# Kernel tuning notes

Hardware: AMD Instinct MI355X
Metric: run time of the kernel (lower is better)

## Reference

```python
import jax, jax.numpy as jnp
import numpy as np

N_NODES = 100000
N_EDGES = 400000
N_GRAPHS = 2048
F_IN = 78
HEADS1 = 10
OUT2 = 128


def _gat_conv(x, src, dst, W, a_src, a_dst, b, heads, out_dim):
    """PyG-style GATConv with self-loops already included in (src, dst)."""
    N = x.shape[0]
    h = (x @ W).reshape(N, heads, out_dim)                       # [N,H,D]
    alpha_src = jnp.einsum('nhd,hd->nh', h, a_src)               # [N,H]
    alpha_dst = jnp.einsum('nhd,hd->nh', h, a_dst)               # [N,H]
    e = jax.nn.leaky_relu(alpha_src[src] + alpha_dst[dst], 0.2)  # [E,H]
    # ragged softmax over incoming edges per destination node
    m = jax.ops.segment_max(e, dst, num_segments=N)
    m = jnp.where(jnp.isfinite(m), m, 0.0)
    ex = jnp.exp(e - jax.lax.stop_gradient(m)[dst])
    denom = jax.ops.segment_sum(ex, dst, num_segments=N)
    alpha = ex / (denom[dst] + 1e-16)                            # [E,H]
    msg = h[src] * alpha[:, :, None]                             # [E,H,D]
    out = jax.ops.segment_sum(msg, dst, num_segments=N)          # [N,H,D]
    return out.reshape(N, heads * out_dim) + b


def setup_inputs() -> dict:
    key = jax.random.key(0)
    ks = jax.random.split(key, 24)
    p = lambda k, shape: (jax.random.normal(k, shape, dtype=jnp.float32) * 0.05)
    x = jax.random.normal(ks[0], (N_NODES, F_IN), dtype=jnp.float32)
    edge_index = jax.random.randint(ks[1], (2, N_EDGES), 0, N_NODES, dtype=jnp.int32)
    # sorted batch assignment guaranteeing every graph is non-empty
    batch = ((jnp.arange(N_NODES, dtype=jnp.int32) * N_GRAPHS) // N_NODES).astype(jnp.int32)
    target = jax.random.normal(ks[2], (N_GRAPHS, 1280), dtype=jnp.float32)
    return {
        'x': x, 'edge_index': edge_index, 'batch': batch, 'target': target,
        'W1': p(ks[3], (F_IN, HEADS1 * F_IN)),
        'a_src1': p(ks[4], (HEADS1, F_IN)),
        'a_dst1': p(ks[5], (HEADS1, F_IN)),
        'b1': jnp.zeros((HEADS1 * F_IN,), jnp.float32),
        'W2': p(ks[6], (HEADS1 * F_IN, OUT2)),
        'a_src2': p(ks[7], (1, OUT2)),
        'a_dst2': p(ks[8], (1, OUT2)),
        'b2': jnp.zeros((OUT2,), jnp.float32),
        'w_gate': p(ks[9], (OUT2, 1)),
        'b_gate': jnp.zeros((1,), jnp.float32),
        'W_xt': p(ks[10], (1280, 256)),
        'b_xt': jnp.zeros((256,), jnp.float32),
        'W_fc1': p(ks[11], (512, 1024)),
        'b_fc1': jnp.zeros((1024,), jnp.float32),
        'W_fc2': p(ks[12], (1024, 256)),
        'b_fc2': jnp.zeros((256,), jnp.float32),
        'W_out': p(ks[13], (256, 1)),
        'b_out': jnp.zeros((1,), jnp.float32),
    }


def reference(x, edge_index, batch, target, W1, a_src1, a_dst1, b1,
              W2, a_src2, a_dst2, b2, w_gate, b_gate, W_xt, b_xt,
              W_fc1, b_fc1, W_fc2, b_fc2, W_out, b_out):
    N = x.shape[0]
    loop = jnp.arange(N, dtype=edge_index.dtype)
    src = jnp.concatenate([edge_index[0], loop])   # add self-loops (PyG default)
    dst = jnp.concatenate([edge_index[1], loop])

    h = jax.nn.elu(_gat_conv(x, src, dst, W1, a_src1, a_dst1, b1, HEADS1, F_IN))
    h = _gat_conv(h, src, dst, W2, a_src2, a_dst2, b2, 1, OUT2)
    h = jax.nn.relu(h)                              # [N,128]

    # WeightedSumAndMax readout
    w = jax.nn.sigmoid(h @ w_gate + b_gate)         # [N,1]
    h_sum = jax.ops.segment_sum(h * w, batch, num_segments=N_GRAPHS)  # [B,128]
    h_max = jax.ops.segment_max(h, batch, num_segments=N_GRAPHS)     # [B,128]
    hg = jnp.concatenate([h_sum, h_max], axis=1)    # [B,256]

    xt = target @ W_xt + b_xt                       # [B,256]
    xc = jnp.concatenate([hg, xt], axis=1)          # [B,512]
    xc = jax.nn.relu(xc @ W_fc1 + b_fc1)
    xc = jax.nn.relu(xc @ W_fc2 + b_fc2)
    return xc @ W_out + b_out                       # [B,1]
```

## Files before the change

kernel.cpp:

```cpp
#include <hip/hip_runtime.h>
#include <cstdint>
#include <cstddef>

#define N_NODESC 100000
#define N_EDGESC 400000
#define N_GRAPHSC 2048
#define F_INC 78
#define HEADS1C 10
#define D1C 78
#define F1C 780
#define OUT2C 128
#define E_TOTC (N_EDGESC + N_NODESC)

typedef unsigned short ushort_t;
typedef __attribute__((ext_vector_type(8))) short short8;
typedef __attribute__((ext_vector_type(4))) float f32x4;
typedef __attribute__((ext_vector_type(4))) unsigned int uint4v;
union U4S8 { uint4v u; short8 s; };

static __device__ __forceinline__ float lrelu(float x){ return x > 0.f ? x : 0.2f*x; }

static __device__ __forceinline__ float elu_fast(float v){
  return (v > 0.f) ? v : (__expf(v) - 1.0f);
}

static __device__ __forceinline__ void bar_lds(){
  asm volatile("s_waitcnt lgkmcnt(0)" ::: "memory");
  __builtin_amdgcn_s_barrier();
}

static __device__ __forceinline__ unsigned short f2bf(float f){
  unsigned int u = __float_as_uint(f);
  unsigned int r = (u + 0x7fffu + ((u >> 16) & 1u)) >> 16;
  return (unsigned short)r;
}
static __device__ __forceinline__ float bf2f(unsigned short h){
  return __uint_as_float(((unsigned int)h) << 16);
}

__global__ void k_deg(const int* __restrict__ ei, int* __restrict__ deg){
  int e = blockIdx.x*256 + threadIdx.x;
  if (e >= E_TOTC) return;
  int dst = (e < N_EDGESC) ? ei[N_EDGESC + e] : (e - N_EDGESC);
  atomicAdd(&deg[dst], 1);
}

__global__ __launch_bounds__(1024) void k_scan1(const int* __restrict__ deg,
                                                int* __restrict__ rowptr,
                                                int* __restrict__ bsum){
  __shared__ int s[1024];
  int t = threadIdx.x, i = blockIdx.x*1024 + t;
  int v = (i < N_NODESC) ? deg[i] : 0;
  s[t] = v; __syncthreads();
  for (int d = 1; d < 1024; d <<= 1){
    int xv = (t >= d) ? s[t-d] : 0;
    __syncthreads();
    s[t] += xv;
    __syncthreads();
  }
  if (i < N_NODESC) rowptr[i+1] = s[t];
  if (t == 1023) bsum[blockIdx.x] = s[t];
}

__global__ void k_scan2(int* __restrict__ bsum, int* __restrict__ rowptr, int nb){
  if (threadIdx.x == 0 && blockIdx.x == 0){
    int run = 0;
    for (int b = 0; b < nb; b++){ int v = bsum[b]; bsum[b] = run; run += v; }
    rowptr[0] = 0;
  }
}

__global__ __launch_bounds__(1024) void k_scan3(int* __restrict__ rowptr,
                                                const int* __restrict__ bsum){
  int i = blockIdx.x*1024 + threadIdx.x;
  if (i < N_NODESC) rowptr[i+1] += bsum[blockIdx.x];
}

__global__ void k_scatter(const int* __restrict__ ei, const int* __restrict__ rowptr,
                          int* __restrict__ cnt, int* __restrict__ esrc){
  int e = blockIdx.x*256 + threadIdx.x;
  if (e >= E_TOTC) return;
  int src, dst;
  if (e < N_EDGESC){ src = ei[e]; dst = ei[N_EDGESC + e]; }
  else { src = dst = e - N_EDGESC; }
  int pos = rowptr[dst] + atomicAdd(&cnt[dst], 1);
  esrc[pos] = src;
}

__global__ void k_wa1(const float* __restrict__ W1, const float* __restrict__ a_src1,
                      const float* __restrict__ a_dst1, float* __restrict__ Wa1){
  int i = blockIdx.x*256 + threadIdx.x;
  if (i >= F_INC*2*HEADS1C) return;
  int d = i / (2*HEADS1C), c = i % (2*HEADS1C);
  const float* a = (c < HEADS1C) ? a_src1 : a_dst1;
  int h = (c < HEADS1C) ? c : c - HEADS1C;
  float s = 0.f;
  for (int j = 0; j < D1C; j++) s += W1[d*F1C + h*D1C + j] * a[h*D1C + j];
  Wa1[d*(2*HEADS1C) + c] = s;
}

__global__ void k_att1(const float* __restrict__ x, const float* __restrict__ Wa1,
                       float* __restrict__ att1){
  int i = blockIdx.x*256 + threadIdx.x;
  if (i >= N_NODESC*2*HEADS1C) return;
  int n = i / (2*HEADS1C), c = i % (2*HEADS1C);
  const float* xr = x + (size_t)n*F_INC;
  float s = 0.f;
  for (int d = 0; d < F_INC; d++) s += xr[d] * Wa1[d*(2*HEADS1C) + c];
  att1[i] = s;
}

__global__ void k_stats1(const float* __restrict__ att1, const int* __restrict__ rowptr,
                         const int* __restrict__ esrc, float* __restrict__ stat1){
  int i = blockIdx.x*256 + threadIdx.x;
  if (i >= N_NODESC*HEADS1C) return;
  int n = i / HEADS1C, h = i % HEADS1C;
  float ad = att1[n*20 + 10 + h];
  int b = rowptr[n], e = rowptr[n+1];
  float m = -1e30f;
  for (int p = b; p < e; p += 4){
    int c = e - p; if (c > 4) c = 4;
    float v[4];
    #pragma unroll
    for (int j = 0; j < 4; j++){ int s = esrc[p + (j < c ? j : 0)]; v[j] = att1[s*20 + h]; }
    #pragma unroll
    for (int j = 0; j < 4; j++) if (j < c) m = fmaxf(m, lrelu(v[j] + ad));
  }
  float den = 0.f;
  for (int p = b; p < e; p += 4){
    int c = e - p; if (c > 4) c = 4;
    float v[4];
    #pragma unroll
    for (int j = 0; j < 4; j++){ int s = esrc[p + (j < c ? j : 0)]; v[j] = att1[s*20 + h]; }
    #pragma unroll
    for (int j = 0; j < 4; j++) if (j < c) den += expf(lrelu(v[j] + ad) - m);
  }
  stat1[n*20 + h] = m;
  stat1[n*20 + 10 + h] = 1.f/(den + 1e-16f);
}

__global__ __launch_bounds__(64) void k_agg1(
    const float* __restrict__ x, const float* __restrict__ att1,
    const float* __restrict__ stat1, const int* __restrict__ rowptr,
    const int* __restrict__ esrc, ushort_t* __restrict__ zc, int base){
  __shared__ float xs[4][F_INC];
  __shared__ float al[4][HEADS1C];
  int n = base + blockIdx.x;
  int l = threadIdx.x;
  int b = rowptr[n], e = rowptr[n+1];
  float acc[13];
  #pragma unroll
  for (int k = 0; k < 13; k++) acc[k] = 0.f;
  int hk[13], dk[13];
  #pragma unroll
  for (int k = 0; k < 13; k++){ int f = l + 64*k; hk[k] = f/78; dk[k] = f%78; }
  float ad = 0.f, mm = 0.f, rd = 0.f;
  if (l < HEADS1C){
    ad = att1[n*20 + 10 + l];
    mm = stat1[n*20 + l];
    rd = stat1[n*20 + 10 + l];
  }
  for (int p = b; p < e; p += 4){
    int c = e - p; if (c > 4) c = 4;
    int ss[4];
    #pragma unroll
    for (int j = 0; j < 4; j++) ss[j] = esrc[p + (j < c ? j : 0)];
    if (l < 39){
      #pragma unroll
      for (int j = 0; j < 4; j++){
        float2 v = *(const float2*)(x + (size_t)ss[j]*F_INC + 2*l);
        xs[j][2*l] = v.x; xs[j][2*l+1] = v.y;
      }
    }
    if (l < HEADS1C){
      #pragma unroll
      for (int j = 0; j < 4; j++){
        float ev = lrelu(att1[ss[j]*20 + l] + ad);
        al[j][l] = (j < c) ? expf(ev - mm) * rd : 0.f;
      }
    }
    __syncthreads();
    #pragma unroll
    for (int k = 0; k < 13; k++){
      int f = l + 64*k;
      if (f < F1C){
        float s = al[0][hk[k]]*xs[0][dk[k]] + al[1][hk[k]]*xs[1][dk[k]]
                + al[2][hk[k]]*xs[2][dk[k]] + al[3][hk[k]]*xs[3][dk[k]];
        acc[k] += s;
      }
    }
    __syncthreads();
  }
  #pragma unroll
  for (int k = 0; k < 13; k++){
    int f = l + 64*k;
    if (f < F1C) zc[(size_t)blockIdx.x*F1C + f] = f2bf(acc[k]);
  }
}

__global__ void k_prepW1(const float* __restrict__ W1, ushort_t* __restrict__ W1t){
  int i = blockIdx.x*256 + threadIdx.x;
  if (i >= HEADS1C*80*96) return;
  int h = i / (80*96), rem = i % (80*96), n = rem / 96, k = rem % 96;
  float v = (n < D1C && k < F_INC) ? W1[(size_t)k*F1C + h*D1C + n] : 0.f;
  W1t[i] = f2bf(v);
}

__global__ void k_prepW2f(const float* __restrict__ W2, ushort_t* __restrict__ W2f){
  int i = blockIdx.x*256 + threadIdx.x;
  if (i >= HEADS1C*128*96) return;
  int h = i / (128*96), rem = i % (128*96), n = rem / 96, k = rem % 96;
  float v = (k < D1C) ? W2[(size_t)(h*D1C + k)*OUT2C + n] : 0.f;
  W2f[i] = f2bf(v);
}

__global__ void k_prepWt(const float* __restrict__ W, ushort_t* __restrict__ Wt,
                         int Kdim, int Ndim, int KB){
  int i = blockIdx.x*256 + threadIdx.x;
  if (i >= Ndim*KB) return;
  int n = i / KB, k = i % KB;
  float v = (k < Kdim) ? W[(size_t)k*Ndim + n] : 0.f;
  Wt[i] = f2bf(v);
}

__global__ void k_cast_bf(const float* __restrict__ in, ushort_t* __restrict__ o, int n){
  int i = blockIdx.x*256 + threadIdx.x;
  if (i < n) o[i] = f2bf(in[i]);
}

template<int BN, int NT, int KB, int KVAL, int ACT, bool HASBIAS>
__global__ __launch_bounds__(256) void mfma_gemm(
    const ushort_t* __restrict__ A, const ushort_t* __restrict__ Bt,
    const float* __restrict__ bias, ushort_t* __restrict__ C,
    int M, int N, int lda, int ldc,
    int zsA, int zsBt, int zsC, int zsBias)
{
  __shared__ unsigned int As[64][20];
  __shared__ unsigned int Bs[BN][20];
  int z = blockIdx.z;
  A += (size_t)z*zsA; Bt += (size_t)z*zsBt; C += (size_t)z*zsC;
  const float* bz = HASBIAS ? (bias + (size_t)z*zsBias) : nullptr;
  int m0 = blockIdx.x*64;
  int n0 = blockIdx.y*BN;
  int t = threadIdx.x;
  int w = t >> 6, lane = t & 63;
  int q = lane >> 4, li = lane & 15;
  f32x4 acc[NT];
  #pragma unroll
  for (int i = 0; i < NT; i++) acc[i] = (f32x4){0.f,0.f,0.f,0.f};

  int am = t >> 2;
  int ak0 = (t & 3)*8;
  int gm = m0 + am;
  bool rv = (gm < M);

  #pragma unroll
  for (int ki = 0; ki < KB/32; ki++){
    const int kt = ki*32;
    int nv;
    if (ki == KB/32 - 1){
      int d = KVAL - ak0; nv = d < 0 ? 0 : (d > 8 ? 8 : d);
    } else nv = 8;
    {
      unsigned u0=0u, u1=0u, u2=0u, u3=0u;
      if (rv && nv > 0){
        const unsigned int* ap = (const unsigned int*)(A + (size_t)gm*lda + kt + ak0);
        u0 = ap[0]; u1 = ap[1]; u2 = ap[2]; u3 = ap[3];
        int ndw = nv >> 1;
        if (ndw < 4) u3 = 0u;
        if (ndw < 3) u2 = 0u;
        if (ndw < 2) u1 = 0u;
      }
      int c0 = (t & 3)*4;
      As[am][c0] = u0; As[am][c0+1] = u1; As[am][c0+2] = u2; As[am][c0+3] = u3;
    }
    for (int g = t; g < BN*4; g += 256){
      int n = g >> 2, c0 = (g & 3)*4;
      const unsigned int* bp = (const unsigned int*)(Bt + (size_t)(n0 + n)*KB + kt + c0*2);
      Bs[n][c0] = bp[0]; Bs[n][c0+1] = bp[1]; Bs[n][c0+2] = bp[2]; Bs[n][c0+3] = bp[3];
    }
    __syncthreads();
    U4S8 a; a.u = *(const uint4v*)&As[w*16 + li][q*4];
    #pragma unroll
    for (int nt = 0; nt < NT; nt++){
      U4S8 b; b.u = *(const uint4v*)&Bs[nt*16 + li][q*4];
      acc[nt] = __builtin_amdgcn_mfma_f32_16x16x32_bf16(a.s, b.s, acc[nt], 0, 0, 0);
    }
    __syncthreads();
  }
  #pragma unroll
  for (int nt = 0; nt < NT; nt++){
    int col = n0 + nt*16 + li;
    if (col >= N) continue;
    float bv = HASBIAS ? bz[col] : 0.f;
    #pragma unroll
    for (int r = 0; r < 4; r++){
      int gmr = m0 + w*16 + q*4 + r;
      if (gmr >= M) continue;
      float v = acc[nt][r] + bv;
      if (ACT == 1) v = fmaxf(v, 0.f);
      else if (ACT == 2) v = (v > 0.f) ? v : (__expf(v) - 1.0f);
      C[(size_t)gmr*ldc + col] = f2bf(v);
    }
  }
}

__global__ __launch_bounds__(256, 4) void mfma_fused12(
    const ushort_t* __restrict__ zc, const ushort_t* __restrict__ W1t,
    const float* __restrict__ b1, const ushort_t* __restrict__ W2f,
    ushort_t* __restrict__ h2pre, float* __restrict__ att2,
    const float* __restrict__ a_src2, const float* __restrict__ a_dst2,
    int M)
{
  __shared__ unsigned int Bs[128][52];
  __shared__ unsigned int Ts[64][52];
  int m0 = blockIdx.x*64;
  int t = threadIdx.x;
  int w = t >> 6, lane = t & 63;
  int q = lane >> 4, li = lane & 15;

  const uint4v* w1v = (const uint4v*)W1t;
  const uint4v* w2v = (const uint4v*)W2f;

  uint4v rw1[4], rw2[6];
  auto issueW1 = [&](int h){
    #pragma unroll
    for (int g0 = 0; g0 < 4; g0++){
      int g = t + g0*256;
      if (g < 960) rw1[g0] = w1v[(size_t)h*960 + g];
    }
  };
  auto writeW1 = [&](){
    #pragma unroll
    for (int g0 = 0; g0 < 4; g0++){
      int g = t + g0*256;
      if (g < 960){
        int n = g/12, c0 = (g%12)*4;
        *(uint4v*)&Bs[n][c0] = rw1[g0];
      }
    }
  };
  auto issueW2 = [&](int h){
    #pragma unroll
    for (int g0 = 0; g0 < 6; g0++)
      rw2[g0] = w2v[(size_t)h*1536 + t + g0*256];
  };
  auto writeW2 = [&](){
    #pragma unroll
    for (int g0 = 0; g0 < 6; g0++){
      int g = t + g0*256;
      int n = g/12, c0 = (g%12)*4;
      *(uint4v*)&Bs[n][c0] = rw2[g0];
    }
  };

  f32x4 acc2[8];
  #pragma unroll
  for (int i = 0; i < 8; i++) acc2[i] = (f32x4){0.f,0.f,0.f,0.f};

  issueW1(0);

  for (int i = t; i < 64*9; i += 256) Ts[i/9][39 + i%9] = 0u;

  int ar = m0 + w*16 + li;
  bool rv = (ar < M);
  const unsigned int* abase = (const unsigned int*)(zc + (size_t)ar*F1C);

  auto lda = [&](int h, uint4v* af){
    af[0] = (uint4v){0u,0u,0u,0u};
    af[1] = (uint4v){0u,0u,0u,0u};
    af[2] = (uint4v){0u,0u,0u,0u};
    if (rv){
      const unsigned int* p = abase + h*39 + q*4;
      af[0][0]=p[0];  af[0][1]=p[1];  af[0][2]=p[2];  af[0][3]=p[3];
      af[1][0]=p[16]; af[1][1]=p[17]; af[1][2]=p[18]; af[1][3]=p[19];
      if (q < 2){
        af[2][0]=p[32]; af[2][1]=p[33]; af[2][2]=p[34]; af[2][3]=p[35];
        if (q == 1) af[2][3] = 0u;
      }
    }
  };

  uint4v acur[3], anxt[3];
  lda(0, acur);

  #pragma unroll 1
  for (int h = 0; h < HEADS1C; h++){
    bar_lds();
    issueW2(h);
    writeW1();
    float bv[5];
    #pragma unroll
    for (int nt = 0; nt < 5; nt++){
      int col = nt*16 + li;
      bv[nt] = (col < D1C) ? b1[h*D1C + col] : 0.f;
    }
    bar_lds();

    f32x4 acc1[5];
    #pragma unroll
    for (int i = 0; i < 5; i++) acc1[i] = (f32x4){0.f,0.f,0.f,0.f};
    #pragma unroll
    for (int ki = 0; ki < 3; ki++){
      U4S8 a; a.u = acur[ki];
      #pragma unroll
      for (int nt = 0; nt < 5; nt++){
        U4S8 b; b.u = *(const uint4v*)&Bs[nt*16 + li][ki*16 + q*4];
        acc1[nt] = __builtin_amdgcn_mfma_f32_16x16x32_bf16(a.s, b.s, acc1[nt], 0, 0, 0);
      }
    }
    #pragma unroll
    for (int nt = 0; nt < 5; nt++){
      int col = nt*16 + li;
      #pragma unroll
      for (int r = 0; r < 4; r++){
        int row = w*16 + q*4 + r;
        float v = elu_fast(acc1[nt][r] + bv[nt]);
        ((ushort_t*)&Ts[row][0])[col] = f2bf(v);
      }
    }
    lda(h+1 < HEADS1C ? h+1 : 0, anxt);

    bar_lds();
    writeW2();
    issueW1(h+1 < HEADS1C ? h+1 : 0);
    bar_lds();

    #pragma unroll
    for (int ki = 0; ki < 3; ki++){
      U4S8 a; a.u = *(const uint4v*)&Ts[w*16 + li][ki*16 + q*4];
      #pragma unroll
      for (int nt = 0; nt < 8; nt++){
        U4S8 b; b.u = *(const uint4v*)&Bs[nt*16 + li][ki*16 + q*4];
        acc2[nt] = __builtin_amdgcn_mfma_f32_16x16x32_bf16(a.s, b.s, acc2[nt], 0, 0, 0);
      }
    }
    acur[0] = anxt[0]; acur[1] = anxt[1]; acur[2] = anxt[2];
  }

  float as2[8], ad2[8];
  #pragma unroll
  for (int nt = 0; nt < 8; nt++){
    int col = nt*16 + li;
    as2[nt] = a_src2[col];
    ad2[nt] = a_dst2[col];
  }
  #pragma unroll
  for (int r = 0; r < 4; r++){
    int gmr = m0 + w*16 + q*4 + r;
    float p0 = 0.f, p1 = 0.f;
    ushort_t hv[8];
    #pragma unroll
    for (int nt = 0; nt < 8; nt++){
      ushort_t hb = f2bf(acc2[nt][r]);
      float vb = bf2f(hb);
      p0 += vb*as2[nt]; p1 += vb*ad2[nt];
      hv[nt] = hb;
    }
    #pragma unroll
    for (int off = 1; off < 16; off <<= 1){
      p0 += __shfl_xor(p0, off);
      p1 += __shfl_xor(p1, off);
    }
    if (gmr < M){
      #pragma unroll
      for (int nt = 0; nt < 8; nt++)
        h2pre[(size_t)gmr*OUT2C + nt*16 + li] = hv[nt];
      if (li == 0){
        att2[(size_t)gmr*2]     = p0;
        att2[(size_t)gmr*2 + 1] = p1;
      }
    }
  }
}

__global__ void k_stats2(const float* __restrict__ att2, const int* __restrict__ rowptr,
                         const int* __restrict__ esrc, float* __restrict__ stat2){
  int n = blockIdx.x*256 + threadIdx.x;
  if (n >= N_NODESC) return;
  float ad = att2[n*2+1];
  int b = rowptr[n], e = rowptr[n+1];
  float m = -1e30f;
  for (int p = b; p < e; p += 4){
    int c = e - p; if (c > 4) c = 4;
    float v[4];
    #pragma unroll
    for (int j = 0; j < 4; j++){ int s = esrc[p + (j < c ? j : 0)]; v[j] = att2[s*2]; }
    #pragma unroll
    for (int j = 0; j < 4; j++) if (j < c) m = fmaxf(m, lrelu(v[j] + ad));
  }
  float den = 0.f;
  for (int p = b; p < e; p += 4){
    int c = e - p; if (c > 4) c = 4;
    float v[4];
    #pragma unroll
    for (int j = 0; j < 4; j++){ int s = esrc[p + (j < c ? j : 0)]; v[j] = att2[s*2]; }
    #pragma unroll
    for (int j = 0; j < 4; j++) if (j < c) den += expf(lrelu(v[j] + ad) - m);
  }
  stat2[n*2] = m;
  stat2[n*2+1] = 1.f/(den + 1e-16f);
}

__global__ void k_agg2(const ushort_t* __restrict__ h2pre,
                       const float* __restrict__ att2,
                       const float* __restrict__ stat2, const int* __restrict__ rowptr,
                       const int* __restrict__ esrc, const float* __restrict__ b2,
                       const float* __restrict__ w_gate, const float* __restrict__ b_gate,
                       float* __restrict__ h2, float* __restrict__ wnode){
  int n = blockIdx.x*4 + (threadIdx.x >> 6);
  int l = threadIdx.x & 63;
  if (n >= N_NODESC) return;
  float ad = att2[n*2+1], m = stat2[n*2], rd = stat2[n*2+1];
  int b = rowptr[n], e = rowptr[n+1];
  float a0 = 0.f, a1 = 0.f;
  for (int p = b; p < e; p += 4){
    int c = e - p; if (c > 4) c = 4;
    int ss[4];
    #pragma unroll
    for (int j = 0; j < 4; j++) ss[j] = esrc[p + (j < c ? j : 0)];
    unsigned u[4]; float at[4];
    #pragma unroll
    for (int j = 0; j < 4; j++) u[j] = *(const unsigned*)(h2pre + (size_t)ss[j]*OUT2C + 2*l);
    #pragma unroll
    for (int j = 0; j < 4; j++) at[j] = att2[ss[j]*2];
    #pragma unroll
    for (int j = 0; j < 4; j++){
      if (j < c){
        float alpha = expf(lrelu(at[j] + ad) - m) * rd;
        a0 += alpha * bf2f((ushort_t)(u[j] & 0xffffu));
        a1 += alpha * bf2f((ushort_t)(u[j] >> 16));
      }
    }
  }
  float v0 = fmaxf(a0 + b2[2*l],   0.f);
  float v1 = fmaxf(a1 + b2[2*l+1], 0.f);
  float2 hv; hv.x = v0; hv.y = v1;
  *(float2*)(h2 + (size_t)n*OUT2C + 2*l) = hv;
  float pp = v0*w_gate[2*l] + v1*w_gate[2*l+1];
  #pragma unroll
  for (int off = 32; off; off >>= 1) pp += __shfl_xor(pp, off);
  if (l == 0) wnode[n] = 1.f/(1.f + expf(-(pp + b_gate[0])));
}

__global__ __launch_bounds__(128) void k_readout(const float* __restrict__ h2,
                                                 const float* __restrict__ wnode,
                                                 const int* __restrict__ batch,
                                                 ushort_t* __restrict__ xcb){
  __shared__ int lohi[2];
  int g = blockIdx.x, t = threadIdx.x;
  if (t == 0){
    int lo = 0, hi = N_NODESC;
    while (lo < hi){ int mid = (lo+hi) >> 1; if (batch[mid] < g) lo = mid+1; else hi = mid; }
    lohi[0] = lo;
    int lo2 = lo; hi = N_NODESC;
    while (lo2 < hi){ int mid = (lo2+hi) >> 1; if (batch[mid] < g+1) lo2 = mid+1; else hi = mid; }
    lohi[1] = lo2;
  }
  __syncthreads();
  int lo = lohi[0], hi = lohi[1];
  float sum = 0.f, mx = 0.f;
  for (int n = lo; n < hi; n++){
    float v = h2[(size_t)n*OUT2C + t];
    sum += v * wnode[n];
    mx = fmaxf(mx, v);
  }
  xcb[(size_t)g*512 + t] = f2bf(sum);
  xcb[(size_t)g*512 + 128 + t] = f2bf(mx);
}

__global__ void k_final(const ushort_t* __restrict__ f2b, const float* __restrict__ W_out,
                        const float* __restrict__ b_out, float* __restrict__ out){
  int g = blockIdx.x*4 + (threadIdx.x >> 6);
  int l = threadIdx.x & 63;
  if (g >= N_GRAPHSC) return;
  float s = 0.f;
  #pragma unroll
  for (int k = 0; k < 4; k++) s += bf2f(f2b[(size_t)g*256 + l + 64*k]) * W_out[l + 64*k];
  #pragma unroll
  for (int off = 32; off; off >>= 1) s += __shfl_xor(s, off);
  if (l == 0) out[g] = s + b_out[0];
}

extern "C" void kernel_launch(void* const* d_in, const int* in_sizes, int n_in,
                              void* d_out, int out_size, void* d_ws, size_t ws_size,
                              hipStream_t stream) {
  const float* x      = (const float*)d_in[0];
  const int*   ei     = (const int*)d_in[1];
  const int*   batch  = (const int*)d_in[2];
  const float* target = (const float*)d_in[3];
  const float* W1     = (const float*)d_in[4];
  const float* a_src1 = (const float*)d_in[5];
  const float* a_dst1 = (const float*)d_in[6];
  const float* b1     = (const float*)d_in[7];
  const float* W2     = (const float*)d_in[8];
  const float* a_src2 = (const float*)d_in[9];
  const float* a_dst2 = (const float*)d_in[10];
  const float* b2     = (const float*)d_in[11];
  const float* w_gate = (const float*)d_in[12];
  const float* b_gate = (const float*)d_in[13];
  const float* W_xt   = (const float*)d_in[14];
  const float* b_xt   = (const float*)d_in[15];
  const float* W_fc1  = (const float*)d_in[16];
  const float* b_fc1  = (const float*)d_in[17];
  const float* W_fc2  = (const float*)d_in[18];
  const float* b_fc2  = (const float*)d_in[19];
  const float* W_out  = (const float*)d_in[20];
  const float* b_out  = (const float*)d_in[21];
  float* out = (float*)d_out;

  const size_t MB = (size_t)1 << 20;
  int C;
  if      (ws_size >= 245*MB) C = 1;
  else if (ws_size >= 150*MB) C = 2;
  else                        C = 4;
  const int R = N_NODESC / C;

  char* p = (char*)d_ws;
  auto carve = [&](size_t bytes) -> char* {
    char* r = p; p += (bytes + 255) & ~(size_t)255; return r;
  };
  int*   deg    = (int*)  carve((size_t)N_NODESC*4);
  int*   rowptr = (int*)  carve((size_t)(N_NODESC+1)*4);
  int*   cnt    = (int*)  carve((size_t)N_NODESC*4);
  int*   esrc   = (int*)  carve((size_t)E_TOTC*4);
  int*   bsum   = (int*)  carve(128*4);
  float* Wa1    = (float*)carve((size_t)F_INC*20*4);
  float* att1   = (float*)carve((size_t)N_NODESC*20*4);
  float* stat1  = (float*)carve((size_t)N_NODESC*20*4);
  float* att2   = (float*)carve((size_t)N_NODESC*2*4);
  float* stat2  = (float*)carve((size_t)N_NODESC*2*4);
  float* wnode  = (float*)carve((size_t)N_NODESC*4);
  ushort_t* W1t   = (ushort_t*)carve((size_t)HEADS1C*80*96*2);
  ushort_t* W2f   = (ushort_t*)carve((size_t)HEADS1C*128*96*2);
  ushort_t* Wxtt  = (ushort_t*)carve((size_t)256*1280*2);
  ushort_t* Wfc1t = (ushort_t*)carve((size_t)1024*512*2);
  ushort_t* Wfc2t = (ushort_t*)carve((size_t)256*1024*2);
  ushort_t* tb    = (ushort_t*)carve((size_t)N_GRAPHSC*1280*2);
  ushort_t* h2pre = (ushort_t*)carve((size_t)N_NODESC*OUT2C*2);
  ushort_t* xcb   = (ushort_t*)carve((size_t)N_GRAPHSC*512*2);
  ushort_t* f1b   = (ushort_t*)carve((size_t)N_GRAPHSC*1024*2);
  ushort_t* f2b   = (ushort_t*)carve((size_t)N_GRAPHSC*256*2);
  size_t big_bytes = (size_t)R*F1C*2 + 4096;
  size_t h2_bytes  = (size_t)N_NODESC*OUT2C*4;
  char*  BIG = carve(big_bytes > h2_bytes ? big_bytes : h2_bytes);
  ushort_t* zc  = (ushort_t*)BIG;
  float* h2 = (float*)BIG;

  hipMemsetAsync(deg, 0, (size_t)N_NODESC*4, stream);
  hipMemsetAsync(cnt, 0, (size_t)N_NODESC*4, stream);

  k_deg<<<(E_TOTC+255)/256, 256, 0, stream>>>(ei, deg);
  int nb = (N_NODESC + 1023)/1024;
  k_scan1<<<nb, 1024, 0, stream>>>(deg, rowptr, bsum);
  k_scan2<<<1, 64, 0, stream>>>(bsum, rowptr, nb);
  k_scan3<<<nb, 1024, 0, stream>>>(rowptr, bsum);
  k_scatter<<<(E_TOTC+255)/256, 256, 0, stream>>>(ei, rowptr, cnt, esrc);

  k_prepW1<<<(HEADS1C*80*96+255)/256, 256, 0, stream>>>(W1, W1t);
  k_prepW2f<<<(HEADS1C*128*96+255)/256, 256, 0, stream>>>(W2, W2f);
  k_prepWt<<<(256*1280+255)/256, 256, 0, stream>>>(W_xt, Wxtt, 1280, 256, 1280);
  k_prepWt<<<(1024*512+255)/256, 256, 0, stream>>>(W_fc1, Wfc1t, 512, 1024, 512);
  k_prepWt<<<(256*1024+255)/256, 256, 0, stream>>>(W_fc2, Wfc2t, 1024, 256, 1024);
  k_cast_bf<<<((N_GRAPHSC*1280)+255)/256, 256, 0, stream>>>(target, tb, N_GRAPHSC*1280);

  k_wa1<<<(F_INC*20+255)/256, 256, 0, stream>>>(W1, a_src1, a_dst1, Wa1);
  k_att1<<<(N_NODESC*20+255)/256, 256, 0, stream>>>(x, Wa1, att1);
  k_stats1<<<(N_NODESC*HEADS1C+255)/256, 256, 0, stream>>>(att1, rowptr, esrc, stat1);

  for (int c = 0; c < C; c++){
    int base = c*R;
    k_agg1<<<R, 64, 0, stream>>>(x, att1, stat1, rowptr, esrc, zc, base);
    mfma_fused12<<<(R+63)/64, 256, 0, stream>>>(
        zc, W1t, b1, W2f, h2pre + (size_t)base*OUT2C, att2 + (size_t)base*2,
        a_src2, a_dst2, R);
  }

  k_stats2<<<(N_NODESC+255)/256, 256, 0, stream>>>(att2, rowptr, esrc, stat2);
  k_agg2<<<(N_NODESC+3)/4, 256, 0, stream>>>(h2pre, att2, stat2, rowptr, esrc,
                                             b2, w_gate, b_gate, h2, wnode);

  k_readout<<<N_GRAPHSC, 128, 0, stream>>>(h2, wnode, batch, xcb);
  mfma_gemm<128,8,1280,32,0,true><<<dim3(N_GRAPHSC/64, 256/128, 1), 256, 0, stream>>>(
      tb, Wxtt, b_xt, xcb + 256, N_GRAPHSC, 256, 1280, 512, 0,0,0,0);
  mfma_gemm<128,8,512,32,1,true><<<dim3(N_GRAPHSC/64, 1024/128, 1), 256, 0, stream>>>(
      xcb, Wfc1t, b_fc1, f1b, N_GRAPHSC, 1024, 512, 1024, 0,0,0,0);
  mfma_gemm<128,8,1024,32,1,true><<<dim3(N_GRAPHSC/64, 256/128, 1), 256, 0, stream>>>(
      f1b, Wfc2t, b_fc2, f2b, N_GRAPHSC, 256, 1024, 256, 0,0,0,0);
  k_final<<<(N_GRAPHSC+3)/4, 256, 0, stream>>>(f2b, W_out, b_out, out);
}
```

Measured before the change: 663.1 us.

## Use one thread per node in att1/stats1, retune fused12 occupancy and order

k_att1 now gives each thread a whole node and computes all 20 attention logits together, reading x with float2 loads. k_stats1 likewise gives each thread one node across all 10 heads, reading each source row's logits as float2 vectors two edges at a time. This cuts repeated esrc/x reads and index math, but leaves fewer threads and more registers per thread. Separately, mfma_fused12's launch-bounds occupancy hint drops from 4 to 3, and the W1 LDS write now comes before the W2 prefetch issue.

```diff
diff --git a/kernel.cpp b/kernel.cpp
--- a/kernel.cpp
+++ b/kernel.cpp
@@ -99,44 +99,100 @@
   Wa1[d*(2*HEADS1C) + c] = s;
 }
 
-__global__ void k_att1(const float* __restrict__ x, const float* __restrict__ Wa1,
-                       float* __restrict__ att1){
-  int i = blockIdx.x*256 + threadIdx.x;
-  if (i >= N_NODESC*2*HEADS1C) return;
-  int n = i / (2*HEADS1C), c = i % (2*HEADS1C);
+__global__ __launch_bounds__(256) void k_att1(const float* __restrict__ x,
+                                              const float* __restrict__ Wa1,
+                                              float* __restrict__ att1){
+  int n = blockIdx.x*256 + threadIdx.x;
+  if (n >= N_NODESC) return;
   const float* xr = x + (size_t)n*F_INC;
-  float s = 0.f;
-  for (int d = 0; d < F_INC; d++) s += xr[d] * Wa1[d*(2*HEADS1C) + c];
-  att1[i] = s;
-}
-
-__global__ void k_stats1(const float* __restrict__ att1, const int* __restrict__ rowptr,
-                         const int* __restrict__ esrc, float* __restrict__ stat1){
-  int i = blockIdx.x*256 + threadIdx.x;
-  if (i >= N_NODESC*HEADS1C) return;
-  int n = i / HEADS1C, h = i % HEADS1C;
-  float ad = att1[n*20 + 10 + h];
+  float acc[20];
+  #pragma unroll
+  for (int c = 0; c < 20; c++) acc[c] = 0.f;
+  for (int d0 = 0; d0 < F_INC; d0 += 2){
+    float2 xv = *(const float2*)(xr + d0);
+    const float* w0 = Wa1 + d0*20;
+    #pragma unroll
+    for (int c = 0; c < 20; c++)
+      acc[c] += xv.x*w0[c] + xv.y*w0[20 + c];
+  }
+  float* o = att1 + (size_t)n*20;
+  #pragma unroll
+  for (int j = 0; j < 10; j++){
+    float2 ov; ov.x = acc[2*j]; ov.y = acc[2*j+1];
+    *(float2*)(o + 2*j) = ov;
+  }
+}
+
+__global__ __launch_bounds__(256) void k_stats1(const float* __restrict__ att1,
+                                                const int* __restrict__ rowptr,
+                                                const int* __restrict__ esrc,
+                                                float* __restrict__ stat1){
+  int n = blockIdx.x*256 + threadIdx.x;
+  if (n >= N_NODESC) return;
+  float ad[10];
+  {
+    const float* a = att1 + (size_t)n*20 + 10;
+    #pragma unroll
+    for (int j = 0; j < 5; j++){
+      float2 v = *(const float2*)(a + 2*j);
+      ad[2*j] = v.x; ad[2*j+1] = v.y;
+    }
+  }
   int b = rowptr[n], e = rowptr[n+1];
-  float m = -1e30f;
-  for (int p = b; p < e; p += 4){
-    int c = e - p; if (c > 4) c = 4;
-    float v[4];
-    #pragma unroll
-    for (int j = 0; j < 4; j++){ int s = esrc[p + (j < c ? j : 0)]; v[j] = att1[s*20 + h]; }
-    #pragma unroll
-    for (int j = 0; j < 4; j++) if (j < c) m = fmaxf(m, lrelu(v[j] + ad));
-  }
-  float den = 0.f;
-  for (int p = b; p < e; p += 4){
-    int c = e - p; if (c > 4) c = 4;
-    float v[4];
-    #pragma unroll
-    for (int j = 0; j < 4; j++){ int s = esrc[p + (j < c ? j : 0)]; v[j] = att1[s*20 + h]; }
-    #pragma unroll
-    for (int j = 0; j < 4; j++) if (j < c) den += expf(lrelu(v[j] + ad) - m);
-  }
-  stat1[n*20 + h] = m;
-  stat1[n*20 + 10 + h] = 1.f/(den + 1e-16f);
+  float m[10];
+  #pragma unroll
+  for (int h = 0; h < 10; h++) m[h] = -1e30f;
+  for (int p = b; p < e; p += 2){
+    int s0 = esrc[p];
+    int s1 = esrc[(p+1 < e) ? p+1 : p];
+    float2 v0[5], v1[5];
+    #pragma unroll
+    for (int j = 0; j < 5; j++) v0[j] = *(const float2*)(att1 + (size_t)s0*20 + 2*j);
+    #pragma unroll
+    for (int j = 0; j < 5; j++) v1[j] = *(const float2*)(att1 + (size_t)s1*20 + 2*j);
+    #pragma unroll
+    for (int h = 0; h < 10; h++){
+      float a0 = (h & 1) ? v0[h>>1].y : v0[h>>1].x;
+      m[h] = fmaxf(m[h], lrelu(a0 + ad[h]));
+    }
+    if (p+1 < e){
+      #pragma unroll
+      for (int h = 0; h < 10; h++){
+        float a1 = (h & 1) ? v1[h>>1].y : v1[h>>1].x;
+        m[h] = fmaxf(m[h], lrelu(a1 + ad[h]));
+      }
+    }
+  }
+  float den[10];
+  #pragma unroll
+  for (int h = 0; h < 10; h++) den[h] = 0.f;
+  for (int p = b; p < e; p += 2){
+    int s0 = esrc[p];
+    int s1 = esrc[(p+1 < e) ? p+1 : p];
+    float2 v0[5], v1[5];
+    #pragma unroll
+    for (int j = 0; j < 5; j++) v0[j] = *(const float2*)(att1 + (size_t)s0*20 + 2*j);
+    #pragma unroll
+    for (int j = 0; j < 5; j++) v1[j] = *(const float2*)(att1 + (size_t)s1*20 + 2*j);
+    #pragma unroll
+    for (int h = 0; h < 10; h++){
+      float a0 = (h & 1) ? v0[h>>1].y : v0[h>>1].x;
+      den[h] += expf(lrelu(a0 + ad[h]) - m[h]);
+    }
+    if (p+1 < e){
+      #pragma unroll
+      for (int h = 0; h < 10; h++){
+        float a1 = (h & 1) ? v1[h>>1].y : v1[h>>1].x;
+        den[h] += expf(lrelu(a1 + ad[h]) - m[h]);
+      }
+    }
+  }
+  float* o = stat1 + (size_t)n*20;
+  #pragma unroll
+  for (int h = 0; h < 10; h++){
+    o[h] = m[h];
+    o[10 + h] = 1.f/(den[h] + 1e-16f);
+  }
 }
 
 __global__ __launch_bounds__(64) void k_agg1(
@@ -305,7 +361,7 @@
   }
 }
 
-__global__ __launch_bounds__(256, 4) void mfma_fused12(
+__global__ __launch_bounds__(256, 3) void mfma_fused12(
     const ushort_t* __restrict__ zc, const ushort_t* __restrict__ W1t,
     const float* __restrict__ b1, const ushort_t* __restrict__ W2f,
     ushort_t* __restrict__ h2pre, float* __restrict__ att2,
@@ -387,8 +443,8 @@
   #pragma unroll 1
   for (int h = 0; h < HEADS1C; h++){
     bar_lds();
+    writeW1();
     issueW2(h);
-    writeW1();
     float bv[5];
     #pragma unroll
     for (int nt = 0; nt < 5; nt++){
@@ -665,8 +721,8 @@
   k_cast_bf<<<((N_GRAPHSC*1280)+255)/256, 256, 0, stream>>>(target, tb, N_GRAPHSC*1280);
 
   k_wa1<<<(F_INC*20+255)/256, 256, 0, stream>>>(W1, a_src1, a_dst1, Wa1);
-  k_att1<<<(N_NODESC*20+255)/256, 256, 0, stream>>>(x, Wa1, att1);
-  k_stats1<<<(N_NODESC*HEADS1C+255)/256, 256, 0, stream>>>(att1, rowptr, esrc, stat1);
+  k_att1<<<(N_NODESC+255)/256, 256, 0, stream>>>(x, Wa1, att1);
+  k_stats1<<<(N_NODESC+255)/256, 256, 0, stream>>>(att1, rowptr, esrc, stat1);
 
   for (int c = 0; c < C; c++){
     int base = c*R;
```

Result: faster. 629.3 us (-5.1%).
